# Kernel tuning notes

Measured on AMD Instinct MI355X. Metric: run time of the kernel, lower is better.

Reference implementation:

```python
import jax, jax.numpy as jnp
import numpy as np

B, S, D, H = 2, 2048, 1024, 16
DH = D // H  # head dim = 64


def setup_inputs() -> dict:
    key = jax.random.key(0)
    ks = jax.random.split(key, 10)
    q = jax.random.normal(ks[0], (B, S, D), dtype=jnp.float32)
    k = jax.random.normal(ks[1], (B, S, D), dtype=jnp.float32)
    v = jax.random.normal(ks[2], (B, S, D), dtype=jnp.float32)
    # causal mask: True = masked (as in masked_fill)
    causal = jnp.triu(jnp.ones((S, S), dtype=bool), k=1)
    mask = jnp.broadcast_to(causal, (B, S, S))
    sc = 1.0 / np.sqrt(D)
    Wv = jax.random.normal(ks[3], (DH, D), dtype=jnp.float32) * sc
    bv = jnp.zeros((DH,), dtype=jnp.float32)
    Wq = jax.random.normal(ks[4], (H, DH, D), dtype=jnp.float32) * sc  # per-head query proj
    bq = jnp.zeros((H, DH), dtype=jnp.float32)
    Wk = jax.random.normal(ks[5], (H, DH, D), dtype=jnp.float32) * sc  # per-head key proj
    bk = jnp.zeros((H, DH), dtype=jnp.float32)
    Wo = jax.random.normal(ks[6], (D, DH), dtype=jnp.float32) * (1.0 / np.sqrt(DH))  # final proj, no bias
    return {"q": q, "k": k, "v": v, "mask": mask,
            "Wv": Wv, "bv": bv, "Wq": Wq, "bq": bq, "Wk": Wk, "bk": bk, "Wo": Wo}


def reference(q, k, v, mask, Wv, bv, Wq, bq, Wk, bk, Wo):
    # shared value projection across heads: [B,S,DH]
    v_proj = jnp.einsum('bsd,ed->bse', v, Wv) + bv
    # per-head Q/K projections, batched over heads: [B,H,S,DH]
    qh = jnp.einsum('bsd,hed->bhse', q, Wq) + bq[None, :, None, :]
    kh = jnp.einsum('bsd,hed->bhse', k, Wk) + bk[None, :, None, :]
    scale = jnp.sqrt(jnp.asarray(DH, dtype=qh.dtype))
    attn = jnp.einsum('bhse,bhte->bhst', qh, kh) / scale  # [B,H,S,S]
    attn = jnp.where(mask[:, None, :, :], jnp.asarray(-1e9, attn.dtype), attn)
    attn = jax.nn.softmax(attn, axis=-1)
    out_h = jnp.einsum('bhst,bte->bhse', attn, v_proj)  # shared V across heads
    mean_head = out_h.mean(axis=1)  # mean over heads: [B,S,DH]
    out = jnp.einsum('bse,de->bsd', mean_head, Wo)  # [B,S,D]
    attn_stacked = jnp.transpose(attn, (0, 2, 1, 3))  # [B,S,H,S] to match torch.stack(dim=2)
    return out, attn_stacked
```

## Files before the change

kernel.cpp:

```cpp
#include <hip/hip_runtime.h>
#include <cstdint>
#include <math.h>

typedef unsigned short u16;
typedef __bf16 bf16x8 __attribute__((ext_vector_type(8)));
typedef float f32x4 __attribute__((ext_vector_type(4)));

constexpr int Bc = 2, Sc = 2048, Dc = 1024, Hc = 16, DHc = 64;

__device__ __forceinline__ u16 f2bf(float f) {
  uint32_t u = __builtin_bit_cast(uint32_t, f);
  u += 0x7fffu + ((u >> 16) & 1u);
  return (u16)(u >> 16);
}
__device__ __forceinline__ float bf2f(u16 h) {
  uint32_t u = ((uint32_t)h) << 16;
  return __builtin_bit_cast(float, u);
}
__device__ __forceinline__ f32x4 mfma16(bf16x8 a, bf16x8 b, f32x4 c) {
  return __builtin_amdgcn_mfma_f32_16x16x32_bf16(a, b, c, 0, 0, 0);
}
__device__ __forceinline__ void gload16(const void* g, void* l) {
  __builtin_amdgcn_global_load_lds((const uint32_t*)g, (uint32_t*)l, 16, 0, 0);
}
__device__ __forceinline__ bf16x8 pk8(f32x4 a, f32x4 b) {
  alignas(16) u16 t[8];
  #pragma unroll
  for (int j = 0; j < 4; ++j) { t[j] = f2bf(a[j]); t[4 + j] = f2bf(b[j]); }
  return *reinterpret_cast<const bf16x8*>(t);
}

__global__ __launch_bounds__(256) void cvt_all(
    const float* __restrict__ q, const float* __restrict__ k, const float* __restrict__ v,
    const float* __restrict__ Wq, const float* __restrict__ Wk,
    const float* __restrict__ Wv, const float* __restrict__ Wo,
    u16* __restrict__ qo, u16* __restrict__ ko, u16* __restrict__ vo,
    u16* __restrict__ Wqo, u16* __restrict__ Wko, u16* __restrict__ Wvo,
    u16* __restrict__ Woo) {
  constexpr int NQ = Bc * Sc * Dc / 4;
  constexpr int NW = Hc * DHc * Dc / 4;
  constexpr int NS = DHc * Dc / 4;
  constexpr int C1 = NQ, C2 = 2 * NQ, C3 = 3 * NQ;
  constexpr int C4 = C3 + NW, C5 = C4 + NW, C6 = C5 + NS, C7 = C6 + NS;
  const int i = blockIdx.x * 256 + threadIdx.x;
  if (i >= C7) return;
  const float* src; u16* dst; int j;
  if (i < C1)      { src = q;  dst = qo;  j = i; }
  else if (i < C2) { src = k;  dst = ko;  j = i - C1; }
  else if (i < C3) { src = v;  dst = vo;  j = i - C2; }
  else if (i < C4) { src = Wq; dst = Wqo; j = i - C3; }
  else if (i < C5) { src = Wk; dst = Wko; j = i - C4; }
  else if (i < C6) { src = Wv; dst = Wvo; j = i - C5; }
  else             { src = Wo; dst = Woo; j = i - C6; }
  float4 x = reinterpret_cast<const float4*>(src)[j];
  ushort4 o;
  o.x = f2bf(x.x); o.y = f2bf(x.y); o.z = f2bf(x.z); o.w = f2bf(x.w);
  reinterpret_cast<ushort4*>(dst)[j] = o;
}

__global__ __launch_bounds__(256) void gemm_qkv(
    const u16* __restrict__ qbf, const u16* __restrict__ kbf, const u16* __restrict__ vbf,
    const u16* __restrict__ Wqb, const u16* __restrict__ Wkb, const u16* __restrict__ Wvb,
    const float* __restrict__ bq, const float* __restrict__ bk, const float* __restrict__ bv,
    float qscale, u16* __restrict__ qh, u16* __restrict__ kh, u16* __restrict__ vT) {
  constexpr int K = 1024;
  const int z = blockIdx.z;
  if (z == 2 && blockIdx.x != 0) return;
  const u16* A  = z == 0 ? qbf : (z == 1 ? kbf : vbf);
  const u16* Bw = z == 0 ? Wqb : (z == 1 ? Wkb : Wvb);
  const float* bias = z == 0 ? bq : (z == 1 ? bk : bv);
  const float scale = z == 0 ? qscale : 1.0f;

  __shared__ u16 As[128 * 32];
  __shared__ u16 Bs[128 * 32];
  const int tid = threadIdx.x;
  const int lane = tid & 63;
  const int w = tid >> 6, wm = w >> 1, wn = w & 1;
  const int lo = lane & 15, hi = lane >> 4;
  const int m0 = blockIdx.y * 128, n0 = blockIdx.x * 128;
  const int r16 = lane >> 2;
  const int c8 = (lane & 3) * 8;
  const f32x4 vzero = {0.f, 0.f, 0.f, 0.f};

  f32x4 acc[4][4];
  #pragma unroll
  for (int i = 0; i < 4; ++i)
    #pragma unroll
    for (int j = 0; j < 4; ++j) acc[i][j] = vzero;

  for (int k0 = 0; k0 < K; k0 += 32) {
    #pragma unroll
    for (int it = 0; it < 2; ++it) {
      const int rg = w * 2 + it;
      const int row = rg * 16 + r16;
      gload16(&A[(long)(m0 + row) * K + k0 + c8], &As[rg * 512]);
      gload16(&Bw[(long)(n0 + row) * K + k0 + c8], &Bs[rg * 512]);
    }
    __syncthreads();
    bf16x8 af[4], bfr[4];
    #pragma unroll
    for (int mi = 0; mi < 4; ++mi)
      af[mi] = *reinterpret_cast<const bf16x8*>(&As[(wm * 64 + mi * 16 + lo) * 32 + hi * 8]);
    #pragma unroll
    for (int nj = 0; nj < 4; ++nj)
      bfr[nj] = *reinterpret_cast<const bf16x8*>(&Bs[(wn * 64 + nj * 16 + lo) * 32 + hi * 8]);
    #pragma unroll
    for (int mi = 0; mi < 4; ++mi)
      #pragma unroll
      for (int nj = 0; nj < 4; ++nj)
        acc[mi][nj] = mfma16(af[mi], bfr[nj], acc[mi][nj]);
    __syncthreads();
  }

  #pragma unroll
  for (int nj = 0; nj < 4; ++nj) {
    const int n = n0 + wn * 64 + nj * 16 + lo;
    if (z == 2 && n >= 64) continue;
    const float bb = bias[n];
    #pragma unroll
    for (int mi = 0; mi < 4; ++mi) {
      #pragma unroll
      for (int r = 0; r < 4; ++r) {
        const int mm = m0 + wm * 64 + mi * 16 + hi * 4 + r;
        const int bidx = mm >> 11, ss = mm & 2047;
        const float val = (acc[mi][nj][r] + bb) * scale;
        if (z < 2) {
          const int hh = n >> 6, ee = n & 63;
          const long idx = bidx * 2097152L + ss * 64L + hh * 131072L + ee;
          (z ? kh : qh)[idx] = f2bf(val);
        } else {
          vT[bidx * 131072L + n * 2048L + ss] = f2bf(val);
        }
      }
    }
  }
}

__global__ __launch_bounds__(256) void gemm_bt(
    const u16* __restrict__ A, const u16* __restrict__ Bw,
    const float* __restrict__ bias, int M, int N, int K, float scale,
    u16* __restrict__ outb, float* __restrict__ outf,
    int DHn, long strideB, long strideS, long strideH, long strideE) {
  __shared__ u16 As[128 * 32];
  __shared__ u16 Bs[128 * 32];
  const int tid = threadIdx.x;
  const int lane = tid & 63;
  const int w = tid >> 6, wm = w >> 1, wn = w & 1;
  const int lo = lane & 15, hi = lane >> 4;
  const int m0 = blockIdx.y * 128, n0 = blockIdx.x * 128;
  const int r16 = lane >> 2;
  const int c8 = (lane & 3) * 8;
  const f32x4 vzero = {0.f, 0.f, 0.f, 0.f};

  f32x4 acc[4][4];
  #pragma unroll
  for (int i = 0; i < 4; ++i)
    #pragma unroll
    for (int j = 0; j < 4; ++j) acc[i][j] = vzero;

  for (int k0 = 0; k0 < K; k0 += 32) {
    #pragma unroll
    for (int it = 0; it < 2; ++it) {
      const int rg = w * 2 + it;
      const int row = rg * 16 + r16;
      gload16(&A[(long)(m0 + row) * K + k0 + c8], &As[rg * 512]);
      gload16(&Bw[(long)(n0 + row) * K + k0 + c8], &Bs[rg * 512]);
    }
    __syncthreads();
    bf16x8 af[4], bfr[4];
    #pragma unroll
    for (int mi = 0; mi < 4; ++mi)
      af[mi] = *reinterpret_cast<const bf16x8*>(&As[(wm * 64 + mi * 16 + lo) * 32 + hi * 8]);
    #pragma unroll
    for (int nj = 0; nj < 4; ++nj)
      bfr[nj] = *reinterpret_cast<const bf16x8*>(&Bs[(wn * 64 + nj * 16 + lo) * 32 + hi * 8]);
    #pragma unroll
    for (int mi = 0; mi < 4; ++mi)
      #pragma unroll
      for (int nj = 0; nj < 4; ++nj)
        acc[mi][nj] = mfma16(af[mi], bfr[nj], acc[mi][nj]);
    __syncthreads();
  }

  #pragma unroll
  for (int nj = 0; nj < 4; ++nj) {
    const int n = n0 + wn * 64 + nj * 16 + lo;
    if (n >= N) continue;
    const float bb = bias ? bias[n] : 0.f;
    const int hh = n / DHn, ee = n % DHn;
    #pragma unroll
    for (int mi = 0; mi < 4; ++mi) {
      #pragma unroll
      for (int r = 0; r < 4; ++r) {
        const int mm = m0 + wm * 64 + mi * 16 + hi * 4 + r;
        const int bidx = mm >> 11, ss = mm & 2047;
        const long idx = bidx * strideB + ss * strideS + hh * strideH + ee * strideE;
        const float val = (acc[mi][nj][r] + bb) * scale;
        if (outf) outf[idx] = val;
        else outb[idx] = f2bf(val);
      }
    }
  }
}

__global__ __launch_bounds__(256) void attn_fused(
    const u16* __restrict__ qh, const u16* __restrict__ kh,
    const u16* __restrict__ vT, u16* __restrict__ outh,
    float* __restrict__ attn_out) {
  __shared__ float pslds[2][4][16][68];
  __shared__ float pofflds[2][4][16];
  const int tid = threadIdx.x;
  const int lane = tid & 63, w = tid >> 6;
  const int lo = lane & 15, hi = lane >> 4;
  const int blk = blockIdx.x;
  const int bhz = blk & 31, sb = blk >> 5;
  const int b = bhz >> 4, h = bhz & 15;
  const long bh = (long)bhz * Sc;
  const long rowstride = (long)Hc * Sc;
  float* aout = attn_out + (long)b * Sc * rowstride + (long)h * Sc;
  float (*pfA)[68] = pslds[0][w];
  float (*pfB)[68] = pslds[1][w];
  float* poffA = pofflds[0][w];
  float* poffB = pofflds[1][w];
  const f32x4 vzero = {0.f, 0.f, 0.f, 0.f};
  const int idx = sb * 4 + w;
  const float M0 = 16.f;

  const int s0A = idx * 16;
  const int s0B = (127 - idx) * 16;
  const int sendA = (s0A + 79) & ~63;
  const int sendB = (s0B + 79) & ~63;
  const int srowA = s0A + hi * 4;
  const int srowB = s0B + hi * 4;
  const int srow2A = s0A + lo;
  const int srow2B = s0B + lo;
  const f32x4 z4 = {0.f, 0.f, 0.f, 0.f};

  bf16x8 qaA0, qaA1, qaB0, qaB1;
  {
    const u16* qpA = &qh[(bh + s0A + lo) * DHc];
    qaA0 = *reinterpret_cast<const bf16x8*>(&qpA[hi * 8]);
    qaA1 = *reinterpret_cast<const bf16x8*>(&qpA[32 + hi * 8]);
    const u16* qpB = &qh[(bh + s0B + lo) * DHc];
    qaB0 = *reinterpret_cast<const bf16x8*>(&qpB[hi * 8]);
    qaB1 = *reinterpret_cast<const bf16x8*>(&qpB[32 + hi * 8]);
  }

  float lrA[4], lrB[4];
  #pragma unroll
  for (int r = 0; r < 4; ++r) { lrA[r] = 0.f; lrB[r] = 0.f; }
  int tfA = sendA, tfB = sendB;

  for (int t0 = 0; t0 < sendB; t0 += 64) {
    bf16x8 kb[4][2];
    #pragma unroll
    for (int c = 0; c < 4; ++c) {
      const u16* kp = &kh[(bh + t0 + c * 16 + lo) * DHc];
      kb[c][0] = *reinterpret_cast<const bf16x8*>(&kp[hi * 8]);
      kb[c][1] = *reinterpret_cast<const bf16x8*>(&kp[32 + hi * 8]);
    }
    if (tfA < Sc) {
      #pragma unroll
      for (int r = 0; r < 4; ++r)
        __builtin_nontemporal_store(
            z4, reinterpret_cast<f32x4*>(aout + (long)(srowA + r) * rowstride + tfA + lo * 4));
      tfA += 64;
    } else if (tfB < Sc) {
      #pragma unroll
      for (int r = 0; r < 4; ++r)
        __builtin_nontemporal_store(
            z4, reinterpret_cast<f32x4*>(aout + (long)(srowB + r) * rowstride + tfB + lo * 4));
      tfB += 64;
    }
    const bool doA = (t0 < sendA);
    __builtin_amdgcn_s_setprio(1);
    {
      const bool fullB = (t0 + 63 <= s0B);
      #pragma unroll
      for (int c = 0; c < 4; ++c) {
        f32x4 z = mfma16(qaB1, kb[c][1], mfma16(qaB0, kb[c][0], vzero));
        #pragma unroll
        for (int r = 0; r < 4; ++r) {
          float e = exp2f(z[r] - M0);
          if (!fullB) e = ((t0 + c * 16 + lo) <= srowB + r) ? e : 0.f;
          lrB[r] += e;
        }
      }
    }
    if (doA) {
      const bool fullA = (t0 + 63 <= s0A);
      #pragma unroll
      for (int c = 0; c < 4; ++c) {
        f32x4 z = mfma16(qaA1, kb[c][1], mfma16(qaA0, kb[c][0], vzero));
        #pragma unroll
        for (int r = 0; r < 4; ++r) {
          float e = exp2f(z[r] - M0);
          if (!fullA) e = ((t0 + c * 16 + lo) <= srowA + r) ? e : 0.f;
          lrA[r] += e;
        }
      }
    }
    __builtin_amdgcn_s_setprio(0);
  }
  #pragma unroll
  for (int r = 0; r < 4; ++r) {
    #pragma unroll
    for (int dd = 1; dd < 16; dd <<= 1) {
      lrA[r] += __shfl_xor(lrA[r], dd);
      lrB[r] += __shfl_xor(lrB[r], dd);
    }
  }
  if (lo == 0) {
    #pragma unroll
    for (int r = 0; r < 4; ++r) {
      poffA[hi * 4 + r] = M0 + __log2f(lrA[r]);
      poffB[hi * 4 + r] = M0 + __log2f(lrB[r]);
    }
  }
  asm volatile("s_waitcnt lgkmcnt(0)" ::: "memory");
  __builtin_amdgcn_sched_barrier(0);
  const float offA = poffA[lo];
  const float offB = poffB[lo];

  f32x4 accoA[4], accoB[4];
  #pragma unroll
  for (int eb = 0; eb < 4; ++eb) { accoA[eb] = vzero; accoB[eb] = vzero; }
  const int r4 = lane >> 4;
  const int c4 = (lane & 15) * 4;

  for (int t0 = 0; t0 < sendB; t0 += 64) {
    bf16x8 kb[4][2];
    #pragma unroll
    for (int c = 0; c < 4; ++c) {
      const u16* kp = &kh[(bh + t0 + c * 16 + lo) * DHc];
      kb[c][0] = *reinterpret_cast<const bf16x8*>(&kp[hi * 8]);
      kb[c][1] = *reinterpret_cast<const bf16x8*>(&kp[32 + hi * 8]);
    }
    const bool doA = (t0 < sendA);
    __builtin_amdgcn_s_setprio(1);
    {
      const bool fullB = (t0 + 63 <= s0B);
      #pragma unroll
      for (int c = 0; c < 4; ++c) {
        f32x4 zt = mfma16(kb[c][1], qaB1, mfma16(kb[c][0], qaB0, vzero));
        f32x4 p;
        #pragma unroll
        for (int r = 0; r < 4; ++r) {
          const float e = exp2f(zt[r] - offB);
          p[r] = (fullB || (t0 + c * 16 + hi * 4 + r <= srow2B)) ? e : 0.f;
        }
        *reinterpret_cast<f32x4*>(&pfB[lo][c * 16 + hi * 4]) = p;
      }
    }
    if (doA) {
      const bool fullA = (t0 + 63 <= s0A);
      #pragma unroll
      for (int c = 0; c < 4; ++c) {
        f32x4 zt = mfma16(kb[c][1], qaA1, mfma16(kb[c][0], qaA0, vzero));
        f32x4 p;
        #pragma unroll
        for (int r = 0; r < 4; ++r) {
          const float e = exp2f(zt[r] - offA);
          p[r] = (fullA || (t0 + c * 16 + hi * 4 + r <= srow2A)) ? e : 0.f;
        }
        *reinterpret_cast<f32x4*>(&pfA[lo][c * 16 + hi * 4]) = p;
      }
    }
    __builtin_amdgcn_s_setprio(0);
    asm volatile("s_waitcnt lgkmcnt(0)" ::: "memory");
    __builtin_amdgcn_sched_barrier(0);
    #pragma unroll
    for (int j = 0; j < 4; ++j) {
      f32x4 v = *reinterpret_cast<const f32x4*>(&pfB[j * 4 + r4][c4]);
      __builtin_nontemporal_store(
          v, reinterpret_cast<f32x4*>(aout + (long)(s0B + j * 4 + r4) * rowstride + t0 + c4));
    }
    if (doA) {
      #pragma unroll
      for (int j = 0; j < 4; ++j) {
        f32x4 v = *reinterpret_cast<const f32x4*>(&pfA[j * 4 + r4][c4]);
        __builtin_nontemporal_store(
            v, reinterpret_cast<f32x4*>(aout + (long)(s0A + j * 4 + r4) * rowstride + t0 + c4));
      }
    }
    bf16x8 vb[4][2];
    const u16* vp = &vT[((long)b * DHc + lo) * Sc + t0 + hi * 8];
    #pragma unroll
    for (int eb = 0; eb < 4; ++eb) {
      vb[eb][0] = *reinterpret_cast<const bf16x8*>(&vp[(long)eb * 16 * Sc]);
      vb[eb][1] = *reinterpret_cast<const bf16x8*>(&vp[(long)eb * 16 * Sc + 32]);
    }
    __builtin_amdgcn_s_setprio(1);
    {
      f32x4 a0 = *reinterpret_cast<const f32x4*>(&pfB[lo][hi * 8]);
      f32x4 a1 = *reinterpret_cast<const f32x4*>(&pfB[lo][hi * 8 + 4]);
      f32x4 a2 = *reinterpret_cast<const f32x4*>(&pfB[lo][32 + hi * 8]);
      f32x4 a3 = *reinterpret_cast<const f32x4*>(&pfB[lo][32 + hi * 8 + 4]);
      bf16x8 pa0 = pk8(a0, a1);
      bf16x8 pa1 = pk8(a2, a3);
      #pragma unroll
      for (int eb = 0; eb < 4; ++eb)
        accoB[eb] = mfma16(pa1, vb[eb][1], mfma16(pa0, vb[eb][0], accoB[eb]));
    }
    if (doA) {
      f32x4 a0 = *reinterpret_cast<const f32x4*>(&pfA[lo][hi * 8]);
      f32x4 a1 = *reinterpret_cast<const f32x4*>(&pfA[lo][hi * 8 + 4]);
      f32x4 a2 = *reinterpret_cast<const f32x4*>(&pfA[lo][32 + hi * 8]);
      f32x4 a3 = *reinterpret_cast<const f32x4*>(&pfA[lo][32 + hi * 8 + 4]);
      bf16x8 pa0 = pk8(a0, a1);
      bf16x8 pa1 = pk8(a2, a3);
      #pragma unroll
      for (int eb = 0; eb < 4; ++eb)
        accoA[eb] = mfma16(pa1, vb[eb][1], mfma16(pa0, vb[eb][0], accoA[eb]));
    }
    __builtin_amdgcn_s_setprio(0);
  }

  #pragma unroll
  for (int eb = 0; eb < 4; ++eb)
    #pragma unroll
    for (int r = 0; r < 4; ++r) {
      outh[(bh + srowA + r) * DHc + eb * 16 + lo] = f2bf(accoA[eb][r]);
      outh[(bh + srowB + r) * DHc + eb * 16 + lo] = f2bf(accoB[eb][r]);
    }

  for (int t0 = tfA; t0 < Sc; t0 += 64) {
    #pragma unroll
    for (int r = 0; r < 4; ++r)
      __builtin_nontemporal_store(
          z4, reinterpret_cast<f32x4*>(aout + (long)(srowA + r) * rowstride + t0 + lo * 4));
  }
  for (int t0 = tfB; t0 < Sc; t0 += 64) {
    #pragma unroll
    for (int r = 0; r < 4; ++r)
      __builtin_nontemporal_store(
          z4, reinterpret_cast<f32x4*>(aout + (long)(srowB + r) * rowstride + t0 + lo * 4));
  }
}

__global__ __launch_bounds__(256) void mean_kernel(const u16* __restrict__ outh,
                                                   u16* __restrict__ meanb) {
  const int idx = blockIdx.x * 256 + threadIdx.x;
  const int bs = idx >> 3;
  const int e0 = (idx & 7) * 8;
  const int b = bs >> 11, s = bs & 2047;
  float acc[8];
  #pragma unroll
  for (int j = 0; j < 8; ++j) acc[j] = 0.f;
  for (int h = 0; h < Hc; ++h) {
    alignas(16) u16 tmp[8];
    *reinterpret_cast<uint4*>(tmp) =
        *reinterpret_cast<const uint4*>(&outh[((long)(b * Hc + h) * Sc + s) * DHc + e0]);
    #pragma unroll
    for (int j = 0; j < 8; ++j) acc[j] += bf2f(tmp[j]);
  }
  alignas(16) u16 o[8];
  #pragma unroll
  for (int j = 0; j < 8; ++j) o[j] = f2bf(acc[j] * 0.0625f);
  *reinterpret_cast<uint4*>(&meanb[(long)bs * DHc + e0]) = *reinterpret_cast<const uint4*>(o);
}

extern "C" void kernel_launch(void* const* d_in, const int* in_sizes, int n_in,
                              void* d_out, int out_size, void* d_ws, size_t ws_size,
                              hipStream_t stream) {
  (void)in_sizes; (void)n_in; (void)out_size; (void)ws_size;
  const float* q  = (const float*)d_in[0];
  const float* k  = (const float*)d_in[1];
  const float* v  = (const float*)d_in[2];
  const float* Wv = (const float*)d_in[4];
  const float* bv = (const float*)d_in[5];
  const float* Wq = (const float*)d_in[6];
  const float* bq = (const float*)d_in[7];
  const float* Wk = (const float*)d_in[8];
  const float* bk = (const float*)d_in[9];
  const float* Wo = (const float*)d_in[10];

  char* ws = (char*)d_ws;
  u16* qbf   = (u16*)(ws + 0);
  u16* kbf   = (u16*)(ws + 8388608);
  u16* vbf   = (u16*)(ws + 16777216);
  u16* Wqbf  = (u16*)(ws + 25165824);
  u16* Wkbf  = (u16*)(ws + 27262976);
  u16* Wvbf  = (u16*)(ws + 29360128);
  u16* Wobf  = (u16*)(ws + 29491200);
  u16* qhb   = (u16*)(ws + 29622272);
  u16* khb   = (u16*)(ws + 38010880);
  u16* vTb   = (u16*)(ws + 46399488);
  u16* outh  = (u16*)(ws + 46923776);
  u16* meanb = (u16*)(ws + 55312384);

  float* outp  = (float*)d_out;
  float* attnp = (float*)d_out + (long)Bc * Sc * Dc;

  cvt_all<<<(3702784 + 255) / 256, 256, 0, stream>>>(
      q, k, v, Wq, Wk, Wv, Wo, qbf, kbf, vbf, Wqbf, Wkbf, Wvbf, Wobf);

  const int M = Bc * Sc;
  const float qscale = 0.125f * 1.4426950408889634f;
  gemm_qkv<<<dim3(8, 32, 3), 256, 0, stream>>>(
      qbf, kbf, vbf, Wqbf, Wkbf, Wvbf, bq, bk, bv, qscale, qhb, khb, vTb);

  attn_fused<<<512, 256, 0, stream>>>(qhb, khb, vTb, outh, attnp);

  mean_kernel<<<128, 256, 0, stream>>>(outh, meanb);

  gemm_bt<<<dim3(8, 32), 256, 0, stream>>>(meanb, Wobf, nullptr, M, 1024, 64, 1.0f,
      nullptr, outp, 1024, 2097152L, 1024L, 0L, 1L);
}
```

Baseline: 235.5 us.

## Split attention key range across wave pairs and double the grid

Each pair of waves now shares one query tile pair and interleaves over 64-wide key blocks, so the number of blocks doubles to 1024 and each wave does half the key loop. Row-sum partials and output accumulators are combined across the wave pair through shared memory with block barriers before the softmax offset and the final bf16 store. This targets better load balance and occupancy on the causal attention kernel, at the cost of extra LDS traffic, two __syncthreads, and reloading Q per wave pair.

```diff
diff --git a/kernel.cpp b/kernel.cpp
--- a/kernel.cpp
+++ b/kernel.cpp
@@ -208,22 +208,21 @@
     const u16* __restrict__ vT, u16* __restrict__ outh,
     float* __restrict__ attn_out) {
   __shared__ float pslds[2][4][16][68];
-  __shared__ float pofflds[2][4][16];
+  __shared__ float lsum[4][2][16];
   const int tid = threadIdx.x;
   const int lane = tid & 63, w = tid >> 6;
   const int lo = lane & 15, hi = lane >> 4;
   const int blk = blockIdx.x;
   const int bhz = blk & 31, sb = blk >> 5;
-  const int b = bhz >> 4, h = bhz & 15;
+  const int b = bhz >> 4, h2 = bhz & 15;
   const long bh = (long)bhz * Sc;
   const long rowstride = (long)Hc * Sc;
-  float* aout = attn_out + (long)b * Sc * rowstride + (long)h * Sc;
+  float* aout = attn_out + (long)b * Sc * rowstride + (long)h2 * Sc;
   float (*pfA)[68] = pslds[0][w];
   float (*pfB)[68] = pslds[1][w];
-  float* poffA = pofflds[0][w];
-  float* poffB = pofflds[1][w];
   const f32x4 vzero = {0.f, 0.f, 0.f, 0.f};
-  const int idx = sb * 4 + w;
+  const int pr = w >> 1, hf = w & 1;
+  const int idx = sb * 2 + pr;
   const float M0 = 16.f;
 
   const int s0A = idx * 16;
@@ -249,9 +248,9 @@
   float lrA[4], lrB[4];
   #pragma unroll
   for (int r = 0; r < 4; ++r) { lrA[r] = 0.f; lrB[r] = 0.f; }
-  int tfA = sendA, tfB = sendB;
-
-  for (int t0 = 0; t0 < sendB; t0 += 64) {
+  int tfA = sendA + hf * 64, tfB = sendB + hf * 64;
+
+  for (int t0 = hf * 64; t0 < sendB; t0 += 128) {
     bf16x8 kb[4][2];
     #pragma unroll
     for (int c = 0; c < 4; ++c) {
@@ -264,13 +263,13 @@
       for (int r = 0; r < 4; ++r)
         __builtin_nontemporal_store(
             z4, reinterpret_cast<f32x4*>(aout + (long)(srowA + r) * rowstride + tfA + lo * 4));
-      tfA += 64;
+      tfA += 128;
     } else if (tfB < Sc) {
       #pragma unroll
       for (int r = 0; r < 4; ++r)
         __builtin_nontemporal_store(
             z4, reinterpret_cast<f32x4*>(aout + (long)(srowB + r) * rowstride + tfB + lo * 4));
-      tfB += 64;
+      tfB += 128;
     }
     const bool doA = (t0 < sendA);
     __builtin_amdgcn_s_setprio(1);
@@ -313,14 +312,14 @@
   if (lo == 0) {
     #pragma unroll
     for (int r = 0; r < 4; ++r) {
-      poffA[hi * 4 + r] = M0 + __log2f(lrA[r]);
-      poffB[hi * 4 + r] = M0 + __log2f(lrB[r]);
-    }
-  }
-  asm volatile("s_waitcnt lgkmcnt(0)" ::: "memory");
-  __builtin_amdgcn_sched_barrier(0);
-  const float offA = poffA[lo];
-  const float offB = poffB[lo];
+      lsum[w][0][hi * 4 + r] = lrA[r];
+      lsum[w][1][hi * 4 + r] = lrB[r];
+    }
+  }
+  __syncthreads();
+  const int pw = w ^ 1;
+  const float offA = M0 + __log2f(lsum[w][0][lo] + lsum[pw][0][lo]);
+  const float offB = M0 + __log2f(lsum[w][1][lo] + lsum[pw][1][lo]);
 
   f32x4 accoA[4], accoB[4];
   #pragma unroll
@@ -328,7 +327,7 @@
   const int r4 = lane >> 4;
   const int c4 = (lane & 15) * 4;
 
-  for (int t0 = 0; t0 < sendB; t0 += 64) {
+  for (int t0 = hf * 64; t0 < sendB; t0 += 128) {
     bf16x8 kb[4][2];
     #pragma unroll
     for (int c = 0; c < 4; ++c) {
@@ -420,17 +419,33 @@
   for (int eb = 0; eb < 4; ++eb)
     #pragma unroll
     for (int r = 0; r < 4; ++r) {
-      outh[(bh + srowA + r) * DHc + eb * 16 + lo] = f2bf(accoA[eb][r]);
-      outh[(bh + srowB + r) * DHc + eb * 16 + lo] = f2bf(accoB[eb][r]);
-    }
-
-  for (int t0 = tfA; t0 < Sc; t0 += 64) {
+      pfA[hi * 4 + r][eb * 16 + lo] = accoA[eb][r];
+      pfB[hi * 4 + r][eb * 16 + lo] = accoB[eb][r];
+    }
+  __syncthreads();
+  {
+    const int w0 = w & ~1;
+    const int s0S = hf ? s0B : s0A;
+    #pragma unroll
+    for (int rr = 0; rr < 4; ++rr) {
+      const int row = rr * 4 + (lane >> 4);
+      const int col = (lane & 15) * 4;
+      f32x4 x = *reinterpret_cast<const f32x4*>(&pslds[hf][w0][row][col]);
+      f32x4 y = *reinterpret_cast<const f32x4*>(&pslds[hf][w0 + 1][row][col]);
+      ushort4 o;
+      o.x = f2bf(x[0] + y[0]); o.y = f2bf(x[1] + y[1]);
+      o.z = f2bf(x[2] + y[2]); o.w = f2bf(x[3] + y[3]);
+      *reinterpret_cast<ushort4*>(&outh[(bh + s0S + row) * DHc + col]) = o;
+    }
+  }
+
+  for (int t0 = tfA; t0 < Sc; t0 += 128) {
     #pragma unroll
     for (int r = 0; r < 4; ++r)
       __builtin_nontemporal_store(
           z4, reinterpret_cast<f32x4*>(aout + (long)(srowA + r) * rowstride + t0 + lo * 4));
   }
-  for (int t0 = tfB; t0 < Sc; t0 += 64) {
+  for (int t0 = tfB; t0 < Sc; t0 += 128) {
     #pragma unroll
     for (int r = 0; r < 4; ++r)
       __builtin_nontemporal_store(
@@ -500,7 +515,7 @@
   gemm_qkv<<<dim3(8, 32, 3), 256, 0, stream>>>(
       qbf, kbf, vbf, Wqbf, Wkbf, Wvbf, bq, bk, bv, qscale, qhb, khb, vTb);
 
-  attn_fused<<<512, 256, 0, stream>>>(qhb, khb, vTb, outh, attnp);
+  attn_fused<<<1024, 256, 0, stream>>>(qhb, khb, vTb, outh, attnp);
 
   mean_kernel<<<128, 256, 0, stream>>>(outh, meanb);
 
```

Result: faster. 225.1 us (-4.4%).
